# Kernel tuning notes

Measured on AMD Instinct MI355X. Metric: run time of the kernel, lower is better.

## Reference

```python
import jax, jax.numpy as jnp
import numpy as np

SEQ_LEN = 4096
EMBED_DIM = 1024
NUM_HEADS = 16  # head_dim = 64


def setup_inputs() -> dict:
    key = jax.random.key(0)
    k0, k1, k2 = jax.random.split(key, 3)
    std = 0.02
    x = jax.random.normal(k0, (SEQ_LEN, EMBED_DIM), dtype=jnp.float32)
    # torch Linear convention: weight [out_features, in_features], y = x @ W.T + b
    W_qkv = jax.random.normal(k1, (3 * EMBED_DIM, EMBED_DIM), dtype=jnp.float32) * std
    b_qkv = jnp.zeros((3 * EMBED_DIM,), dtype=jnp.float32)
    W_out = jax.random.normal(k2, (EMBED_DIM, EMBED_DIM), dtype=jnp.float32) * std
    b_out = jnp.zeros((EMBED_DIM,), dtype=jnp.float32)
    return {"input": x, "W_qkv": W_qkv, "b_qkv": b_qkv, "W_out": W_out, "b_out": b_out}


def reference(input, W_qkv, b_qkv, W_out, b_out):
    S, E = input.shape
    H = NUM_HEADS
    Dh = E // H
    # fused QKV projection: [S, 3E]
    projected = input @ W_qkv.T + b_qkv
    q, k, v = jnp.split(projected, 3, axis=1)          # each [S, E]
    q = q.reshape(S, H, Dh)
    k = k.reshape(S, H, Dh)
    v = v.reshape(S, H, Dh)
    # unscaled attention (the original applies no 1/sqrt(d) scaling)
    scores = jnp.einsum('shd,thd->hst', q, k)          # [H, S, S] -- full matrix in HBM
    probs = jax.nn.softmax(scores, axis=-1)
    out = jnp.einsum('hst,thd->shd', probs, v)         # [S, H, Dh]
    out = out.reshape(S, E)
    return out @ W_out.T + b_out
```

## Files before the change

### kernel.cpp

```cpp
#include <hip/hip_runtime.h>

typedef unsigned short u16;
typedef short    bf16x8 __attribute__((ext_vector_type(8)));
typedef u16      u16x8  __attribute__((ext_vector_type(8)));
typedef u16      u16x4  __attribute__((ext_vector_type(4)));
typedef float    f32x4  __attribute__((ext_vector_type(4)));
typedef unsigned u32x2  __attribute__((ext_vector_type(2)));

__device__ __forceinline__ u16 f2bf(float f) {
  unsigned x = __float_as_uint(f);
  unsigned r = x + 0x7fffu + ((x >> 16) & 1u);
  return (u16)(r >> 16);
}
__device__ __forceinline__ float bf2f(u16 u) {
  return __uint_as_float(((unsigned)u) << 16);
}
__device__ __forceinline__ float exp2v(float x) {
  float r;
  asm("v_exp_f32 %0, %1" : "=v"(r) : "v"(x));
  return r;
}

__global__ __launch_bounds__(256) void cast3(const float* __restrict__ x,
                                             const float* __restrict__ wq,
                                             const float* __restrict__ wo,
                                             u16* __restrict__ xb,
                                             u16* __restrict__ wqb,
                                             u16* __restrict__ wob) {
  int b = blockIdx.x;
  const float* s; u16* d; int i;
  if (b < 4096)      { s = x;  d = xb;  i = b * 256 + threadIdx.x; }
  else if (b < 7168) { s = wq; d = wqb; i = (b - 4096) * 256 + threadIdx.x; }
  else               { s = wo; d = wob; i = (b - 7168) * 256 + threadIdx.x; }
  f32x4 v = ((const f32x4*)s)[i];
  u16x4 o;
  o[0] = f2bf(v[0]); o[1] = f2bf(v[1]); o[2] = f2bf(v[2]); o[3] = f2bf(v[3]);
  ((u16x4*)d)[i] = o;
}

template<int N, int K, bool OUTF32, bool SCALEQ, bool VSPLIT>
__global__ __launch_bounds__(256) void gemm_bt(const u16* __restrict__ A,
                                               const u16* __restrict__ B,
                                               const float* __restrict__ bias,
                                               void* __restrict__ Cout,
                                               u16* __restrict__ vtout) {
  __shared__ __align__(16) u16 smem[16384];
  const int tid = threadIdx.x;
  const int flat = blockIdx.y * gridDim.x + blockIdx.x;
  const int q8 = (gridDim.x * gridDim.y) >> 3;
  const int sw = (flat & 7) * q8 + (flat >> 3);
  const int m0 = (sw / gridDim.x) * 128, n0 = (sw % gridDim.x) * 128;
  const int wave = tid >> 6, lane = tid & 63;
  const int c = lane & 15, g = lane >> 4;
  const int wm = (wave >> 1) * 64, wn = (wave & 1) * 64;
  f32x4 acc[4][4] = {};

  const int sr = wave * 16 + (lane >> 2);
  const int sc = (lane & 3) * 8;

  auto stage = [&](int buf, int k0) {
#pragma unroll
    for (int j = 0; j < 2; j++) {
      __builtin_amdgcn_global_load_lds(
        (const __attribute__((address_space(1))) void*)(A + (size_t)(m0 + j * 64 + sr) * K + k0 + sc),
        (__attribute__((address_space(3))) void*)&smem[buf * 4096 + (j * 64 + wave * 16) * 32], 16, 0, 0);
      __builtin_amdgcn_global_load_lds(
        (const __attribute__((address_space(1))) void*)(B + (size_t)(n0 + j * 64 + sr) * K + k0 + sc),
        (__attribute__((address_space(3))) void*)&smem[8192 + buf * 4096 + (j * 64 + wave * 16) * 32], 16, 0, 0);
    }
  };

  stage(0, 0);
  __syncthreads();

  const int nT = K / 32;
  for (int t = 0; t < nT; ++t) {
    const int buf = t & 1;
    if (t + 1 < nT) stage(buf ^ 1, (t + 1) * 32);
    bf16x8 af[4], bfr[4];
#pragma unroll
    for (int m = 0; m < 4; m++)
      af[m]  = *(const bf16x8*)&smem[buf * 4096 + (wm + m * 16 + c) * 32 + g * 8];
#pragma unroll
    for (int n = 0; n < 4; n++)
      bfr[n] = *(const bf16x8*)&smem[8192 + buf * 4096 + (wn + n * 16 + c) * 32 + g * 8];
#pragma unroll
    for (int m = 0; m < 4; m++)
#pragma unroll
      for (int n = 0; n < 4; n++)
        acc[m][n] = __builtin_amdgcn_mfma_f32_16x16x32_bf16(af[m], bfr[n], acc[m][n], 0, 0, 0);
    __syncthreads();
  }

  if (VSPLIT && n0 >= 2048) {
#pragma unroll
    for (int n = 0; n < 4; n++) {
      float bv = bias[n0 + wn + n * 16 + c];
#pragma unroll
      for (int m = 0; m < 4; m++) {
#pragma unroll
        for (int r = 0; r < 4; r++) {
          int nl = wn + n * 16 + c;
          int ml = wm + m * 16 + g * 4 + r;
          int Gs = (ml >> 3) ^ (nl & 15);
          smem[nl * 128 + (Gs << 3) + (ml & 7)] = f2bf(acc[m][n][r] + bv);
        }
      }
    }
    __syncthreads();
    const int nl = tid >> 1, half = tid & 1;
    const int hd = n0 - 2048 + nl;
    u16* dst = vtout + (size_t)hd * 4096 + m0 + half * 64;
#pragma unroll
    for (int Gj = 0; Gj < 8; Gj++) {
      int G = half * 8 + Gj;
      u16x8 v = *(const u16x8*)&smem[nl * 128 + ((G ^ (nl & 15)) << 3)];
      *(u16x8*)(dst + Gj * 8) = v;
    }
    return;
  }

  const float qscale = (SCALEQ && n0 < 1024) ? 1.44269504f : 1.0f;
#pragma unroll
  for (int n = 0; n < 4; n++) {
    float bv = bias[n0 + wn + n * 16 + c];
#pragma unroll
    for (int m = 0; m < 4; m++) {
#pragma unroll
      for (int r = 0; r < 4; r++) {
        float val = (acc[m][n][r] + bv) * qscale;
        int row = m0 + wm + m * 16 + g * 4 + r;
        int col = n0 + wn + n * 16 + c;
        if constexpr (OUTF32) ((float*)Cout)[(size_t)row * N + col] = val;
        else                  ((u16*)Cout)[(size_t)row * N + col] = f2bf(val);
      }
    }
  }
}

__global__ __launch_bounds__(256, 4) void attn_kernel(const u16* __restrict__ qkv,
                                                      const u16* __restrict__ vt,
                                                      u16* __restrict__ pb0,
                                                      u16* __restrict__ pb1,
                                                      float* __restrict__ lb0,
                                                      float* __restrict__ lb1) {
  const int bid0 = blockIdx.x;
  const int bid  = (bid0 & 7) * 128 + (bid0 >> 3);
  const int kk  = bid & 1;
  const int qt  = (bid >> 1) & 31;
  const int h   = bid >> 6;
  const int q0  = qt * 128;
  const int kbase = kk * 2048;
  const int tid = threadIdx.x;
  const int wave = tid >> 6, lane = tid & 63;
  const int c = lane & 15, g = lane >> 4;
  const int qw = q0 + wave * 32;

  __shared__ __align__(16) u16 kls[2][64 * 64];
  __shared__ __align__(16) u16 vls[2][64 * 64];
  __shared__ __align__(16) unsigned plds[4][16 * 32];
  unsigned* pw = plds[wave];
  const int pswz = (c & 7) << 2;

  const u16* Kg = qkv + 1024 + h * 64;
  const u16* Vg = vt + (size_t)h * 64 * 4096;

  const int srow = lane >> 3, sgr = lane & 7;
  const int gc = sgr ^ (srow & 7);
  const u16* kp = Kg + (size_t)(kbase + wave * 16 + srow) * 3072 + gc * 8;
  const u16* vp = Vg + (size_t)(wave * 16 + srow) * 4096 + kbase + gc * 8;

  auto stage = [&](int buf, const u16* kpp, const u16* vpp) {
#pragma unroll
    for (int j = 0; j < 2; j++) {
      __builtin_amdgcn_global_load_lds(
        (const __attribute__((address_space(1))) void*)(kpp + (size_t)j * 8 * 3072),
        (__attribute__((address_space(3))) void*)&kls[buf][(wave * 16 + j * 8) * 64], 16, 0, 0);
      __builtin_amdgcn_global_load_lds(
        (const __attribute__((address_space(1))) void*)(vpp + (size_t)j * 8 * 4096),
        (__attribute__((address_space(3))) void*)&vls[buf][(wave * 16 + j * 8) * 64], 16, 0, 0);
    }
  };

  bf16x8 qf[2][2];
#pragma unroll
  for (int qs = 0; qs < 2; qs++)
#pragma unroll
    for (int dc = 0; dc < 2; dc++)
      qf[qs][dc] = *(const bf16x8*)&qkv[(size_t)(qw + qs * 16 + c) * 3072 + h * 64 + dc * 32 + g * 8];

  bf16x8 ones;
#pragma unroll
  for (int j = 0; j < 8; j++) ones[j] = (short)0x3F80;

  f32x4 o0[4] = {}, o1[4] = {};
  f32x4 accl0 = {}, accl1 = {};
  const f32x4 minit = {-16.f, -16.f, -16.f, -16.f};

  auto softmax = [&](f32x4 (&st)[4]) {
#pragma unroll
    for (int ks = 0; ks < 4; ks++) {
      float p0 = exp2v(st[ks][0]), p1 = exp2v(st[ks][1]);
      float p2 = exp2v(st[ks][2]), p3 = exp2v(st[ks][3]);
      unsigned w0, w1;
      asm("v_cvt_pk_bf16_f32 %0, %1, %2" : "=v"(w0) : "v"(p0), "v"(p1));
      asm("v_cvt_pk_bf16_f32 %0, %1, %2" : "=v"(w1) : "v"(p2), "v"(p3));
      u32x2 w2 = {w0, w1};
      *(u32x2*)&pw[c * 32 + ((ks * 8 + g * 2) ^ pswz)] = w2;
    }
  };

  stage(0, kp, vp);
  kp += (size_t)64 * 3072; vp += 64;
  __syncthreads();

  for (int t = 0; t < 32; ++t) {
    const int buf = t & 1;
    if (t + 1 < 32) {
      stage(buf ^ 1, kp, vp);
      kp += (size_t)64 * 3072; vp += 64;
    }

    f32x4 st0[4], st1[4];
    __builtin_amdgcn_s_setprio(1);
#pragma unroll
    for (int ks = 0; ks < 4; ks++) {
      bf16x8 kf0 = *(const bf16x8*)&kls[buf][(ks * 16 + c) * 64 + ((g ^ (c & 7)) << 3)];
      bf16x8 kf1 = *(const bf16x8*)&kls[buf][(ks * 16 + c) * 64 + (((4 + g) ^ (c & 7)) << 3)];
      f32x4 s0 = __builtin_amdgcn_mfma_f32_16x16x32_bf16(kf0, qf[0][0], minit, 0, 0, 0);
      st0[ks]  = __builtin_amdgcn_mfma_f32_16x16x32_bf16(kf1, qf[0][1], s0, 0, 0, 0);
      f32x4 s1 = __builtin_amdgcn_mfma_f32_16x16x32_bf16(kf0, qf[1][0], minit, 0, 0, 0);
      st1[ks]  = __builtin_amdgcn_mfma_f32_16x16x32_bf16(kf1, qf[1][1], s1, 0, 0, 0);
    }
    __builtin_amdgcn_s_setprio(0);

    softmax(st0);
    bf16x8 pa0[2], pa1[2];
#pragma unroll
    for (int hh = 0; hh < 2; hh++)
      pa0[hh] = *(const bf16x8*)&pw[c * 32 + ((hh * 16 + g * 4) ^ pswz)];
    softmax(st1);
#pragma unroll
    for (int hh = 0; hh < 2; hh++)
      pa1[hh] = *(const bf16x8*)&pw[c * 32 + ((hh * 16 + g * 4) ^ pswz)];

    __builtin_amdgcn_s_setprio(1);
#pragma unroll
    for (int k2 = 0; k2 < 2; k2++) {
      accl0 = __builtin_amdgcn_mfma_f32_16x16x32_bf16(pa0[k2], ones, accl0, 0, 0, 0);
      accl1 = __builtin_amdgcn_mfma_f32_16x16x32_bf16(pa1[k2], ones, accl1, 0, 0, 0);
#pragma unroll
      for (int dt = 0; dt < 4; dt++) {
        bf16x8 vf = *(const bf16x8*)&vls[buf][(dt * 16 + c) * 64 + (((k2 * 4 + g) ^ (c & 7)) << 3)];
        o0[dt] = __builtin_amdgcn_mfma_f32_16x16x32_bf16(pa0[k2], vf, o0[dt], 0, 0, 0);
        o1[dt] = __builtin_amdgcn_mfma_f32_16x16x32_bf16(pa1[k2], vf, o1[dt], 0, 0, 0);
      }
    }
    __builtin_amdgcn_s_setprio(0);
    __syncthreads();
  }

  u16* pb = kk ? pb1 : pb0;
  float* lb = (kk ? lb1 : lb0) + h * 4096 + qw;
  u16* pq = pb + (size_t)qw * 1024 + h * 64;

#pragma unroll
  for (int r = 0; r < 4; r++) {
    int rl = g * 4 + r;
    float inv0 = 1.0f / accl0[r];
    float inv1 = 1.0f / accl1[r];
#pragma unroll
    for (int dt = 0; dt < 4; dt++) {
      pq[(size_t)rl * 1024 + dt * 16 + c]        = f2bf(o0[dt][r] * inv0);
      pq[(size_t)(16 + rl) * 1024 + dt * 16 + c] = f2bf(o1[dt][r] * inv1);
    }
    if (c == 0) {
      lb[rl]      = accl0[r];
      lb[16 + rl] = accl1[r];
    }
  }
}

__global__ __launch_bounds__(256) void combine_kernel(u16* __restrict__ pb0,
                                                      const u16* __restrict__ pb1,
                                                      const float* __restrict__ lb0,
                                                      const float* __restrict__ lb1) {
  int t = blockIdx.x * 256 + threadIdx.x;
  int q = t >> 7;
  int c8 = t & 127;
  int h = c8 >> 3;
  float A = lb0[h * 4096 + q];
  float B = lb1[h * 4096 + q];
  float inv = 1.0f / (A + B);
  float w0 = A * inv, w1 = B * inv;
  size_t off = (size_t)q * 1024 + c8 * 8;
  u16x8 x0 = *(const u16x8*)(pb0 + off);
  u16x8 x1 = *(const u16x8*)(pb1 + off);
  u16x8 o;
#pragma unroll
  for (int e = 0; e < 8; e++)
    o[e] = f2bf(bf2f(x0[e]) * w0 + bf2f(x1[e]) * w1);
  *(u16x8*)(pb0 + off) = o;
}

extern "C" void kernel_launch(void* const* d_in, const int* in_sizes, int n_in,
                              void* d_out, int out_size, void* d_ws, size_t ws_size,
                              hipStream_t stream) {
  const float* x    = (const float*)d_in[0];
  const float* Wqkv = (const float*)d_in[1];
  const float* bqkv = (const float*)d_in[2];
  const float* Wout = (const float*)d_in[3];
  const float* bout = (const float*)d_in[4];

  char* ws = (char*)d_ws;
  u16* xb    = (u16*)(ws);
  u16* wqkvb = (u16*)(ws + (size_t)8  * (1u << 20));
  u16* woutb = (u16*)(ws + (size_t)14 * (1u << 20));
  u16* qkvb  = (u16*)(ws + (size_t)16 * (1u << 20));
  u16* vtb   = (u16*)(ws + (size_t)40 * (1u << 20));
  u16* pb0   = (u16*)(ws + (size_t)48 * (1u << 20));
  char* dob = (char*)d_out;
  u16*   pb1 = (u16*)dob;
  float* lb0 = (float*)(dob + (size_t)8 * (1u << 20));
  float* lb1 = lb0 + 65536;

  cast3<<<8192, 256, 0, stream>>>(x, Wqkv, Wout, xb, wqkvb, woutb);

  gemm_bt<3072, 1024, false, true, true><<<dim3(24, 32), 256, 0, stream>>>(
      xb, wqkvb, bqkv, qkvb, vtb);

  attn_kernel<<<1024, 256, 0, stream>>>(qkvb, vtb, pb0, pb1, lb0, lb1);

  combine_kernel<<<2048, 256, 0, stream>>>(pb0, pb1, lb0, lb1);

  gemm_bt<1024, 1024, true, false, false><<<dim3(8, 32), 256, 0, stream>>>(
      pb0, woutb, bout, d_out, nullptr);
}
```

Baseline: 170.2 us.

## Enlarge attention query tile to 64 rows per wave with 4-way KV split

Each attention block now handles 256 queries (64 per wave) over a quarter of the keys instead of 128 queries over half, so each K/V tile staged in LDS feeds twice as many MFMAs. The grid size stays the same, and the combine kernel now merges four partial outputs using their row sums. Partial buffers reuse freed workspace (the bf16 x and W_qkv casts) and the output buffer. The cost is doubled accumulator registers per wave, which may lower occupancy or cause spills, plus extra combine traffic.

New measurement: 550.2 us. 3.23x slower.

```diff
diff --git a/kernel.cpp b/kernel.cpp
--- a/kernel.cpp
+++ b/kernel.cpp
@@ -142,19 +142,20 @@
                                                       const u16* __restrict__ vt,
                                                       u16* __restrict__ pb0,
                                                       u16* __restrict__ pb1,
-                                                      float* __restrict__ lb0,
-                                                      float* __restrict__ lb1) {
+                                                      u16* __restrict__ pb2,
+                                                      u16* __restrict__ pb3,
+                                                      float* __restrict__ lball) {
   const int bid0 = blockIdx.x;
   const int bid  = (bid0 & 7) * 128 + (bid0 >> 3);
-  const int kk  = bid & 1;
-  const int qt  = (bid >> 1) & 31;
+  const int kk  = bid & 3;
+  const int qt  = (bid >> 2) & 15;
   const int h   = bid >> 6;
-  const int q0  = qt * 128;
-  const int kbase = kk * 2048;
+  const int q0  = qt * 256;
+  const int kbase = kk * 1024;
   const int tid = threadIdx.x;
   const int wave = tid >> 6, lane = tid & 63;
   const int c = lane & 15, g = lane >> 4;
-  const int qw = q0 + wave * 32;
+  const int qw = q0 + wave * 64;
 
   __shared__ __align__(16) u16 kls[2][64 * 64];
   __shared__ __align__(16) u16 vls[2][64 * 64];
@@ -182,9 +183,9 @@
     }
   };
 
-  bf16x8 qf[2][2];
-#pragma unroll
-  for (int qs = 0; qs < 2; qs++)
+  bf16x8 qf[4][2];
+#pragma unroll
+  for (int qs = 0; qs < 4; qs++)
 #pragma unroll
     for (int dc = 0; dc < 2; dc++)
       qf[qs][dc] = *(const bf16x8*)&qkv[(size_t)(qw + qs * 16 + c) * 3072 + h * 64 + dc * 32 + g * 8];
@@ -193,8 +194,8 @@
 #pragma unroll
   for (int j = 0; j < 8; j++) ones[j] = (short)0x3F80;
 
-  f32x4 o0[4] = {}, o1[4] = {};
-  f32x4 accl0 = {}, accl1 = {};
+  f32x4 o[4][4] = {};
+  f32x4 accl[4] = {};
   const f32x4 minit = {-16.f, -16.f, -16.f, -16.f};
 
   auto softmax = [&](f32x4 (&st)[4]) {
@@ -214,92 +215,97 @@
   kp += (size_t)64 * 3072; vp += 64;
   __syncthreads();
 
-  for (int t = 0; t < 32; ++t) {
+  for (int t = 0; t < 16; ++t) {
     const int buf = t & 1;
-    if (t + 1 < 32) {
+    if (t + 1 < 16) {
       stage(buf ^ 1, kp, vp);
       kp += (size_t)64 * 3072; vp += 64;
     }
 
-    f32x4 st0[4], st1[4];
+    f32x4 st[4][4];
     __builtin_amdgcn_s_setprio(1);
 #pragma unroll
     for (int ks = 0; ks < 4; ks++) {
       bf16x8 kf0 = *(const bf16x8*)&kls[buf][(ks * 16 + c) * 64 + ((g ^ (c & 7)) << 3)];
       bf16x8 kf1 = *(const bf16x8*)&kls[buf][(ks * 16 + c) * 64 + (((4 + g) ^ (c & 7)) << 3)];
-      f32x4 s0 = __builtin_amdgcn_mfma_f32_16x16x32_bf16(kf0, qf[0][0], minit, 0, 0, 0);
-      st0[ks]  = __builtin_amdgcn_mfma_f32_16x16x32_bf16(kf1, qf[0][1], s0, 0, 0, 0);
-      f32x4 s1 = __builtin_amdgcn_mfma_f32_16x16x32_bf16(kf0, qf[1][0], minit, 0, 0, 0);
-      st1[ks]  = __builtin_amdgcn_mfma_f32_16x16x32_bf16(kf1, qf[1][1], s1, 0, 0, 0);
+#pragma unroll
+      for (int qs = 0; qs < 4; qs++) {
+        f32x4 s = __builtin_amdgcn_mfma_f32_16x16x32_bf16(kf0, qf[qs][0], minit, 0, 0, 0);
+        st[qs][ks] = __builtin_amdgcn_mfma_f32_16x16x32_bf16(kf1, qf[qs][1], s, 0, 0, 0);
+      }
     }
     __builtin_amdgcn_s_setprio(0);
 
-    softmax(st0);
-    bf16x8 pa0[2], pa1[2];
-#pragma unroll
-    for (int hh = 0; hh < 2; hh++)
-      pa0[hh] = *(const bf16x8*)&pw[c * 32 + ((hh * 16 + g * 4) ^ pswz)];
-    softmax(st1);
-#pragma unroll
-    for (int hh = 0; hh < 2; hh++)
-      pa1[hh] = *(const bf16x8*)&pw[c * 32 + ((hh * 16 + g * 4) ^ pswz)];
+    bf16x8 pa[4][2];
+#pragma unroll
+    for (int qs = 0; qs < 4; qs++) {
+      softmax(st[qs]);
+#pragma unroll
+      for (int hh = 0; hh < 2; hh++)
+        pa[qs][hh] = *(const bf16x8*)&pw[c * 32 + ((hh * 16 + g * 4) ^ pswz)];
+    }
 
     __builtin_amdgcn_s_setprio(1);
 #pragma unroll
     for (int k2 = 0; k2 < 2; k2++) {
-      accl0 = __builtin_amdgcn_mfma_f32_16x16x32_bf16(pa0[k2], ones, accl0, 0, 0, 0);
-      accl1 = __builtin_amdgcn_mfma_f32_16x16x32_bf16(pa1[k2], ones, accl1, 0, 0, 0);
+#pragma unroll
+      for (int qs = 0; qs < 4; qs++)
+        accl[qs] = __builtin_amdgcn_mfma_f32_16x16x32_bf16(pa[qs][k2], ones, accl[qs], 0, 0, 0);
 #pragma unroll
       for (int dt = 0; dt < 4; dt++) {
         bf16x8 vf = *(const bf16x8*)&vls[buf][(dt * 16 + c) * 64 + (((k2 * 4 + g) ^ (c & 7)) << 3)];
-        o0[dt] = __builtin_amdgcn_mfma_f32_16x16x32_bf16(pa0[k2], vf, o0[dt], 0, 0, 0);
-        o1[dt] = __builtin_amdgcn_mfma_f32_16x16x32_bf16(pa1[k2], vf, o1[dt], 0, 0, 0);
+#pragma unroll
+        for (int qs = 0; qs < 4; qs++)
+          o[qs][dt] = __builtin_amdgcn_mfma_f32_16x16x32_bf16(pa[qs][k2], vf, o[qs][dt], 0, 0, 0);
       }
     }
     __builtin_amdgcn_s_setprio(0);
     __syncthreads();
   }
 
-  u16* pb = kk ? pb1 : pb0;
-  float* lb = (kk ? lb1 : lb0) + h * 4096 + qw;
+  u16* pb = (kk == 0) ? pb0 : (kk == 1) ? pb1 : (kk == 2) ? pb2 : pb3;
+  float* lb = lball + kk * 65536 + h * 4096 + qw;
   u16* pq = pb + (size_t)qw * 1024 + h * 64;
 
 #pragma unroll
-  for (int r = 0; r < 4; r++) {
-    int rl = g * 4 + r;
-    float inv0 = 1.0f / accl0[r];
-    float inv1 = 1.0f / accl1[r];
-#pragma unroll
-    for (int dt = 0; dt < 4; dt++) {
-      pq[(size_t)rl * 1024 + dt * 16 + c]        = f2bf(o0[dt][r] * inv0);
-      pq[(size_t)(16 + rl) * 1024 + dt * 16 + c] = f2bf(o1[dt][r] * inv1);
-    }
-    if (c == 0) {
-      lb[rl]      = accl0[r];
-      lb[16 + rl] = accl1[r];
+  for (int qs = 0; qs < 4; qs++) {
+#pragma unroll
+    for (int r = 0; r < 4; r++) {
+      int rl = g * 4 + r;
+      float inv = 1.0f / accl[qs][r];
+#pragma unroll
+      for (int dt = 0; dt < 4; dt++)
+        pq[(size_t)(qs * 16 + rl) * 1024 + dt * 16 + c] = f2bf(o[qs][dt][r] * inv);
+      if (c == 0) lb[qs * 16 + rl] = accl[qs][r];
     }
   }
 }
 
 __global__ __launch_bounds__(256) void combine_kernel(u16* __restrict__ pb0,
                                                       const u16* __restrict__ pb1,
-                                                      const float* __restrict__ lb0,
-                                                      const float* __restrict__ lb1) {
+                                                      const u16* __restrict__ pb2,
+                                                      const u16* __restrict__ pb3,
+                                                      const float* __restrict__ lball) {
   int t = blockIdx.x * 256 + threadIdx.x;
   int q = t >> 7;
   int c8 = t & 127;
   int h = c8 >> 3;
-  float A = lb0[h * 4096 + q];
-  float B = lb1[h * 4096 + q];
-  float inv = 1.0f / (A + B);
-  float w0 = A * inv, w1 = B * inv;
+  int ri = h * 4096 + q;
+  float l0 = lball[ri];
+  float l1 = lball[65536 + ri];
+  float l2 = lball[131072 + ri];
+  float l3 = lball[196608 + ri];
+  float inv = 1.0f / (l0 + l1 + l2 + l3);
+  float w0 = l0 * inv, w1 = l1 * inv, w2 = l2 * inv, w3 = l3 * inv;
   size_t off = (size_t)q * 1024 + c8 * 8;
   u16x8 x0 = *(const u16x8*)(pb0 + off);
   u16x8 x1 = *(const u16x8*)(pb1 + off);
+  u16x8 x2 = *(const u16x8*)(pb2 + off);
+  u16x8 x3 = *(const u16x8*)(pb3 + off);
   u16x8 o;
 #pragma unroll
   for (int e = 0; e < 8; e++)
-    o[e] = f2bf(bf2f(x0[e]) * w0 + bf2f(x1[e]) * w1);
+    o[e] = f2bf(bf2f(x0[e]) * w0 + bf2f(x1[e]) * w1 + bf2f(x2[e]) * w2 + bf2f(x3[e]) * w3);
   *(u16x8*)(pb0 + off) = o;
 }
 
@@ -319,19 +325,20 @@
   u16* qkvb  = (u16*)(ws + (size_t)16 * (1u << 20));
   u16* vtb   = (u16*)(ws + (size_t)40 * (1u << 20));
   u16* pb0   = (u16*)(ws + (size_t)48 * (1u << 20));
+  u16*   pb1   = xb;
+  float* lball = (float*)wqkvb;
   char* dob = (char*)d_out;
-  u16*   pb1 = (u16*)dob;
-  float* lb0 = (float*)(dob + (size_t)8 * (1u << 20));
-  float* lb1 = lb0 + 65536;
+  u16* pb2 = (u16*)dob;
+  u16* pb3 = (u16*)(dob + (size_t)8 * (1u << 20));
 
   cast3<<<8192, 256, 0, stream>>>(x, Wqkv, Wout, xb, wqkvb, woutb);
 
   gemm_bt<3072, 1024, false, true, true><<<dim3(24, 32), 256, 0, stream>>>(
       xb, wqkvb, bqkv, qkvb, vtb);
 
-  attn_kernel<<<1024, 256, 0, stream>>>(qkvb, vtb, pb0, pb1, lb0, lb1);
-
-  combine_kernel<<<2048, 256, 0, stream>>>(pb0, pb1, lb0, lb1);
+  attn_kernel<<<1024, 256, 0, stream>>>(qkvb, vtb, pb0, pb1, pb2, pb3, lball);
+
+  combine_kernel<<<2048, 256, 0, stream>>>(pb0, pb1, pb2, pb3, lball);
 
   gemm_bt<1024, 1024, true, false, false><<<dim3(8, 32), 256, 0, stream>>>(
       pb0, woutb, bout, d_out, nullptr);
```
